# Kernel optimization log

Hardware: AMD Instinct MI355X
Metric: run time of the kernel (lower is better)

The kernel has to match this reference:

```python
import jax, jax.numpy as jnp
import numpy as np

FACTOR = 4  # 2 ** n_downsample
EPS = 1e-6


def _resize_bilinear(x, oh, ow):
    # F.interpolate(mode='bilinear', align_corners=False). x: [N,C,H,W]
    N, C, H, W = x.shape
    ys = (jnp.arange(oh, dtype=x.dtype) + 0.5) * (H / oh) - 0.5
    xs = (jnp.arange(ow, dtype=x.dtype) + 0.5) * (W / ow) - 0.5
    y0f = jnp.floor(ys); x0f = jnp.floor(xs)
    wy = (ys - y0f).reshape(1, 1, oh, 1)
    wx = (xs - x0f).reshape(1, 1, 1, ow)
    y0 = jnp.clip(y0f.astype(jnp.int32), 0, H - 1)
    y1 = jnp.clip(y0f.astype(jnp.int32) + 1, 0, H - 1)
    x0 = jnp.clip(x0f.astype(jnp.int32), 0, W - 1)
    x1 = jnp.clip(x0f.astype(jnp.int32) + 1, 0, W - 1)
    g = lambda yi, xi: x[:, :, yi][:, :, :, xi]
    top = g(y0, x0) * (1 - wx) + g(y0, x1) * wx
    bot = g(y1, x0) * (1 - wx) + g(y1, x1) * wx
    return top * (1 - wy) + bot * wy


def _grid_sample_zeros(x, grid):
    # F.grid_sample bilinear, padding_mode='zeros', align_corners=False.
    # x: [N,C,H,W], grid: [N,H,W,2] with (x,y) in [-1,1]
    N, C, H, W = x.shape
    px = ((grid[..., 0] + 1.0) * W - 1.0) * 0.5
    py = ((grid[..., 1] + 1.0) * H - 1.0) * 0.5
    x0 = jnp.floor(px).astype(jnp.int32)
    y0 = jnp.floor(py).astype(jnp.int32)
    wx = (px - x0)[:, None]  # [N,1,H,W]
    wy = (py - y0)[:, None]
    xf = x.reshape(N, C, H * W)

    def gather(yi, xi):
        valid = ((yi >= 0) & (yi < H) & (xi >= 0) & (xi < W)).astype(x.dtype)[:, None]
        idx = (jnp.clip(yi, 0, H - 1) * W + jnp.clip(xi, 0, W - 1)).reshape(N, 1, -1)
        v = jnp.take_along_axis(xf, jnp.broadcast_to(idx, (N, C, idx.shape[-1])), axis=2)
        return v.reshape(N, C, yi.shape[1], yi.shape[2]) * valid

    v00 = gather(y0, x0); v01 = gather(y0, x0 + 1)
    v10 = gather(y0 + 1, x0); v11 = gather(y0 + 1, x0 + 1)
    return (v00 * (1 - wx) * (1 - wy) + v01 * wx * (1 - wy)
            + v10 * (1 - wx) * wy + v11 * wx * wy)


def _warp_feature_map(fmap, flow):
    # resize_flow (with component scaling) + grid build + grid_sample
    N, C, H, W = fmap.shape
    rf = _resize_bilinear(flow, H, W)
    scale = jnp.array([W / flow.shape[3], H / flow.shape[2]], dtype=fmap.dtype).reshape(1, 2, 1, 1)
    rf = rf * scale
    gy, gx = jnp.meshgrid(jnp.arange(H, dtype=fmap.dtype), jnp.arange(W, dtype=fmap.dtype), indexing='ij')
    gxn = 2.0 * (gx[None] + rf[:, 0]) / (W - 1) - 1.0
    gyn = 2.0 * (gy[None] + rf[:, 1]) / (H - 1) - 1.0
    grid = jnp.stack([gxn, gyn], axis=-1)  # [N,H,W,2]
    return _grid_sample_zeros(fmap, grid)


def _upsample_flow(flow, mask, factor):
    # convex combination upsampling: unfold 3x3 + softmax over 9 neighbors
    N, D, H, W = flow.shape
    m = jax.nn.softmax(mask.reshape(N, 1, 9, factor, factor, H, W), axis=2)
    fp = jnp.pad(factor * flow, ((0, 0), (0, 0), (1, 1), (1, 1)))
    # 9 shifted views, row-major kernel order to match F.unfold
    nb = jnp.stack([fp[:, :, dy:dy + H, dx:dx + W]
                    for dy in range(3) for dx in range(3)], axis=2)  # [N,D,9,H,W]
    up = jnp.sum(m * nb[:, :, :, None, None], axis=2)  # [N,D,f,f,H,W]
    up = up.transpose(0, 1, 4, 2, 5, 3)  # [N,D,H,f,W,f]
    return up.reshape(N, D, factor * H, factor * W)


def setup_inputs() -> dict:
    key = jax.random.key(0)
    ks = jax.random.split(key, 7)
    N, C, H, W = 8, 256, 192, 320
    FH, FW = 768, 1280
    return {
        'fmap1': jax.random.normal(ks[0], (N, C, H, W), jnp.float32),
        'fmap1_next': jax.random.normal(ks[1], (N, C, H, W), jnp.float32),
        'flow_left': jax.random.normal(ks[2], (N, 2, FH, FW), jnp.float32) * 4.0,
        'mask1': jax.random.uniform(ks[3], (N, 1, FH, FW), jnp.float32),
        'mask1_next': jax.random.uniform(ks[4], (N, 1, FH, FW), jnp.float32),
        'coarse_flow': jax.random.normal(ks[5], (N, 2, H, W), jnp.float32) * 2.0,
        'up_mask': jax.random.normal(ks[6], (N, 9 * FACTOR * FACTOR, H, W), jnp.float32),
    }


def reference(fmap1, fmap1_next, flow_left, mask1, mask1_next, coarse_flow, up_mask):
    N, C, H, W = fmap1.shape
    # warp next-frame features into current frame
    warped = _warp_feature_map(fmap1_next, flow_left)
    # resize soft masks to feature resolution; warp next-frame mask
    rm1 = _resize_bilinear(mask1, H, W)
    rm1n = _warp_feature_map(_resize_bilinear(mask1_next, H, W), flow_left)
    s = rm1 + rm1n
    s = jnp.where(s == 0, jnp.full_like(s, EPS), s)
    fused = (rm1 * fmap1 + rm1n * warped) / s
    # convex upsample of coarse flow, keep disparity channel only
    flow_up = _upsample_flow(coarse_flow, up_mask, FACTOR)[:, :1]
    return fused, flow_up
```

## Files before the change

kernel.cpp:

```cpp
#include <hip/hip_runtime.h>
#include <math.h>

namespace {
constexpr int N_ = 8;
constexpr int C_ = 256;
constexpr int H_ = 192;
constexpr int W_ = 320;
constexpr int SH = 768;
constexpr int SW = 1280;
constexpr int HW = H_ * W_;
constexpr long long FUSED_SIZE = (long long)N_ * C_ * HW;
}

__global__ __launch_bounds__(W_) void fuse_kernel(
    const float* __restrict__ fmap1, const float* __restrict__ fmap1_next,
    const float* __restrict__ flow_left, const float* __restrict__ mask1,
    const float* __restrict__ mask1_next, float* __restrict__ out) {
  int nby = blockIdx.x;
  int n = nby / H_;
  int y = nby % H_;
  int x = threadIdx.x;

  const int sy = 4 * y + 1;
  const int sx = 4 * x + 1;
  const size_t sbase = (size_t)sy * SW + sx;

  const float* fl = flow_left + (size_t)n * 2 * SH * SW;
  const float* flx = fl;
  const float* fly = fl + (size_t)SH * SW;
  float rfx = 0.25f * (0.5f * (0.5f * flx[sbase] + 0.5f * flx[sbase + 1]) +
                       0.5f * (0.5f * flx[sbase + SW] + 0.5f * flx[sbase + SW + 1]));
  float rfy = 0.25f * (0.5f * (0.5f * fly[sbase] + 0.5f * fly[sbase + 1]) +
                       0.5f * (0.5f * fly[sbase + SW] + 0.5f * fly[sbase + SW + 1]));

  float px = (x + rfx) * (320.0f / 319.0f) - 0.5f;
  float py = (y + rfy) * (192.0f / 191.0f) - 0.5f;
  float x0f = floorf(px), y0f = floorf(py);
  int x0 = (int)x0f, y0 = (int)y0f;
  float wx = px - x0f, wy = py - y0f;
  int x1 = x0 + 1, y1 = y0 + 1;
  bool vx0 = (x0 >= 0) & (x0 < W_), vx1 = (x1 >= 0) & (x1 < W_);
  bool vy0 = (y0 >= 0) & (y0 < H_), vy1 = (y1 >= 0) & (y1 < H_);
  int cx0 = min(max(x0, 0), W_ - 1), cx1 = min(max(x1, 0), W_ - 1);
  int cy0 = min(max(y0, 0), H_ - 1), cy1 = min(max(y1, 0), H_ - 1);
  int o00 = cy0 * W_ + cx0, o01 = cy0 * W_ + cx1;
  int o10 = cy1 * W_ + cx0, o11 = cy1 * W_ + cx1;
  float w00 = (vy0 && vx0) ? (1.0f - wx) * (1.0f - wy) : 0.0f;
  float w01 = (vy0 && vx1) ? wx * (1.0f - wy) : 0.0f;
  float w10 = (vy1 && vx0) ? (1.0f - wx) * wy : 0.0f;
  float w11 = (vy1 && vx1) ? wx * wy : 0.0f;

  const float* m1 = mask1 + (size_t)n * SH * SW;
  float rm1 = 0.5f * (0.5f * m1[sbase] + 0.5f * m1[sbase + 1]) +
              0.5f * (0.5f * m1[sbase + SW] + 0.5f * m1[sbase + SW + 1]);

  const float* m1n = mask1_next + (size_t)n * SH * SW;
  auto rmn_at = [&](int yy, int xx) -> float {
    size_t b = (size_t)(4 * yy + 1) * SW + (4 * xx + 1);
    return 0.5f * (0.5f * m1n[b] + 0.5f * m1n[b + 1]) +
           0.5f * (0.5f * m1n[b + SW] + 0.5f * m1n[b + SW + 1]);
  };
  float rm1n = w00 * rmn_at(cy0, cx0) + w01 * rmn_at(cy0, cx1) +
               w10 * rmn_at(cy1, cx0) + w11 * rmn_at(cy1, cx1);

  float s = rm1 + rm1n;
  if (s == 0.0f) s = 1e-6f;
  float a = rm1 / s;
  float b = rm1n / s;
  float bw00 = b * w00, bw01 = b * w01, bw10 = b * w10, bw11 = b * w11;

  const float* f1 = fmap1 + (size_t)n * C_ * HW + y * W_ + x;
  const float* f2 = fmap1_next + (size_t)n * C_ * HW;
  float* o = out + (size_t)n * C_ * HW + y * W_ + x;

#pragma unroll 4
  for (int c = 0; c < C_; ++c) {
    const float* p = f2 + (size_t)c * HW;
    float v1 = f1[(size_t)c * HW];
    float wv = bw00 * p[o00] + bw01 * p[o01] + bw10 * p[o10] + bw11 * p[o11];
    o[(size_t)c * HW] = a * v1 + wv;
  }
}

__global__ __launch_bounds__(W_) void upsample_kernel(
    const float* __restrict__ coarse_flow, const float* __restrict__ up_mask,
    float* __restrict__ out) {
  int b = blockIdx.x;
  int h = b % H_;
  b /= H_;
  int fy = b & 3;
  int n = b >> 2;
  int w = threadIdx.x;

  const float* f = coarse_flow + (size_t)n * 2 * HW;
  float nb[9];
#pragma unroll
  for (int dy = 0; dy < 3; ++dy) {
#pragma unroll
    for (int dx = 0; dx < 3; ++dx) {
      int yy = h + dy - 1, xx = w + dx - 1;
      nb[dy * 3 + dx] = (yy >= 0 && yy < H_ && xx >= 0 && xx < W_)
                            ? 4.0f * f[yy * W_ + xx]
                            : 0.0f;
    }
  }

  const float* mb = up_mask + ((size_t)n * 144 * H_ + (size_t)h) * W_ + w;
  float4 res;
  float* resp = &res.x;
#pragma unroll
  for (int fx = 0; fx < 4; ++fx) {
    int cbase = fy * 4 + fx;
    float mv[9];
#pragma unroll
    for (int k = 0; k < 9; ++k)
      mv[k] = mb[(size_t)(k * 16 + cbase) * HW];
    float mx = mv[0];
#pragma unroll
    for (int k = 1; k < 9; ++k) mx = fmaxf(mx, mv[k]);
    float sum = 0.0f, acc = 0.0f;
#pragma unroll
    for (int k = 0; k < 9; ++k) {
      float e = __expf(mv[k] - mx);
      sum += e;
      acc += e * nb[k];
    }
    resp[fx] = acc / sum;
  }
  float* orow = out + (size_t)(n * SH + 4 * h + fy) * SW;
  *(float4*)(orow + 4 * w) = res;
}

extern "C" void kernel_launch(void* const* d_in, const int* in_sizes, int n_in,
                              void* d_out, int out_size, void* d_ws,
                              size_t ws_size, hipStream_t stream) {
  const float* fmap1 = (const float*)d_in[0];
  const float* fmap1_next = (const float*)d_in[1];
  const float* flow_left = (const float*)d_in[2];
  const float* mask1 = (const float*)d_in[3];
  const float* mask1_next = (const float*)d_in[4];
  const float* coarse_flow = (const float*)d_in[5];
  const float* up_mask = (const float*)d_in[6];
  float* out = (float*)d_out;

  fuse_kernel<<<N_ * H_, W_, 0, stream>>>(fmap1, fmap1_next, flow_left, mask1,
                                          mask1_next, out);
  upsample_kernel<<<N_ * 4 * H_, W_, 0, stream>>>(coarse_flow, up_mask,
                                                  out + FUSED_SIZE);
}
```

Baseline: 1.571 ms.

## Split fuse kernel over channel chunks with XCD-aware block swizzle and nontemporal streaming

The fuse kernel now runs as 64-thread workgroups, each covering a 64-pixel row segment and a 64-channel chunk, instead of one 320-thread block per row looping over all 256 channels. This gives many more workgroups and a shorter serial channel loop per thread. A block-ID swizzle spreads consecutive logical blocks across the 8 XCDs. The streaming fmap1 reads and the output writes use nontemporal hints so they keep the gathered fmap1_next rows in cache. The trade-off is that the flow, mask and warp-weight setup is now recomputed once per channel chunk, four times per pixel.

```diff
diff --git a/kernel.cpp b/kernel.cpp
--- a/kernel.cpp
+++ b/kernel.cpp
@@ -10,16 +10,26 @@
 constexpr int SW = 1280;
 constexpr int HW = H_ * W_;
 constexpr long long FUSED_SIZE = (long long)N_ * C_ * HW;
+
+constexpr int CCHUNK = 64;
+constexpr int NCC = C_ / CCHUNK;
+constexpr int XBLK = W_ / 64;
+constexpr int FUSE_NWG = NCC * N_ * H_ * XBLK;
 }
 
-__global__ __launch_bounds__(W_) void fuse_kernel(
+__global__ __launch_bounds__(64) void fuse_kernel(
     const float* __restrict__ fmap1, const float* __restrict__ fmap1_next,
     const float* __restrict__ flow_left, const float* __restrict__ mask1,
     const float* __restrict__ mask1_next, float* __restrict__ out) {
-  int nby = blockIdx.x;
-  int n = nby / H_;
-  int y = nby % H_;
-  int x = threadIdx.x;
+  int bid = blockIdx.x;
+  int lid = (bid & 7) * (FUSE_NWG / 8) + (bid >> 3);
+  int xb = lid % XBLK;
+  int r = lid / XBLK;
+  int y = r % H_;
+  int t = r / H_;
+  int n = t & 7;
+  int cc = t >> 3;
+  int x = xb * 64 + threadIdx.x;
 
   const int sy = 4 * y + 1;
   const int sx = 4 * x + 1;
@@ -69,16 +79,17 @@
   float b = rm1n / s;
   float bw00 = b * w00, bw01 = b * w01, bw10 = b * w10, bw11 = b * w11;
 
-  const float* f1 = fmap1 + (size_t)n * C_ * HW + y * W_ + x;
-  const float* f2 = fmap1_next + (size_t)n * C_ * HW;
-  float* o = out + (size_t)n * C_ * HW + y * W_ + x;
+  const int c0 = cc * CCHUNK;
+  const float* f1 = fmap1 + ((size_t)n * C_ + c0) * HW + y * W_ + x;
+  const float* f2 = fmap1_next + ((size_t)n * C_ + c0) * HW;
+  float* o = out + ((size_t)n * C_ + c0) * HW + y * W_ + x;
 
-#pragma unroll 4
-  for (int c = 0; c < C_; ++c) {
+#pragma unroll 8
+  for (int c = 0; c < CCHUNK; ++c) {
     const float* p = f2 + (size_t)c * HW;
-    float v1 = f1[(size_t)c * HW];
+    float v1 = __builtin_nontemporal_load(&f1[(size_t)c * HW]);
     float wv = bw00 * p[o00] + bw01 * p[o01] + bw10 * p[o10] + bw11 * p[o11];
-    o[(size_t)c * HW] = a * v1 + wv;
+    __builtin_nontemporal_store(a * v1 + wv, &o[(size_t)c * HW]);
   }
 }
 
@@ -143,8 +154,8 @@
   const float* up_mask = (const float*)d_in[6];
   float* out = (float*)d_out;
 
-  fuse_kernel<<<N_ * H_, W_, 0, stream>>>(fmap1, fmap1_next, flow_left, mask1,
-                                          mask1_next, out);
+  fuse_kernel<<<FUSE_NWG, 64, 0, stream>>>(fmap1, fmap1_next, flow_left, mask1,
+                                           mask1_next, out);
   upsample_kernel<<<N_ * 4 * H_, W_, 0, stream>>>(coarse_flow, up_mask,
                                                   out + FUSED_SIZE);
 }
```

New measurement: 1.511 ms. 3.8% less time.
